# Optimization experiments

Measured on AMD Instinct MI355X. Metric: run time of the kernel, lower is better.

## Reference

```python
import jax, jax.numpy as jnp
from jax import lax
import numpy as np

H = W = 768
N_BOXES = 512
C1, C2 = 32, 64
POOL = 5
NUM_CLASSES = 4
BN_EPS = 1e-5


def setup_inputs() -> dict:
    key = jax.random.key(0)
    ks = jax.random.split(key, 20)
    image = jax.random.normal(ks[0], (1, 3, H, W), jnp.float32)
    # valid boxes: xmax>xmin, ymax>ymin, inside [0, W)
    xmin = jax.random.randint(ks[1], (N_BOXES,), 0, W - 256)
    ymin = jax.random.randint(ks[2], (N_BOXES,), 0, H - 256)
    bw = jax.random.randint(ks[3], (N_BOXES,), 8, 256)
    bh = jax.random.randint(ks[4], (N_BOXES,), 8, 256)
    boxes = jnp.stack([xmin, ymin, xmin + bw, ymin + bh], axis=1).astype(jnp.int32)
    conv1_w = jax.random.normal(ks[5], (C1, 3, 3, 3), jnp.float32) * 0.1
    conv1_b = jax.random.normal(ks[6], (C1,), jnp.float32) * 0.01
    bn1_g = 1.0 + 0.1 * jax.random.normal(ks[7], (C1,), jnp.float32)
    bn1_b = 0.1 * jax.random.normal(ks[8], (C1,), jnp.float32)
    bn1_m = 0.1 * jax.random.normal(ks[9], (C1,), jnp.float32)
    bn1_v = jax.random.uniform(ks[10], (C1,), jnp.float32, 0.5, 1.5)
    conv2_w = jax.random.normal(ks[11], (C2, C1, 3, 3), jnp.float32) * 0.05
    conv2_b = jax.random.normal(ks[12], (C2,), jnp.float32) * 0.01
    bn2_g = 1.0 + 0.1 * jax.random.normal(ks[13], (C2,), jnp.float32)
    bn2_b = 0.1 * jax.random.normal(ks[14], (C2,), jnp.float32)
    bn2_m = 0.1 * jax.random.normal(ks[15], (C2,), jnp.float32)
    bn2_v = jax.random.uniform(ks[16], (C2,), jnp.float32, 0.5, 1.5)
    fc1_w = jax.random.normal(ks[17], (128, C2 * POOL * POOL), jnp.float32) * 0.02
    fc1_b = jnp.zeros((128,), jnp.float32)
    fc2_w = jax.random.normal(ks[18], (NUM_CLASSES, 128), jnp.float32) * 0.05
    fc2_b = jnp.zeros((NUM_CLASSES,), jnp.float32)
    return dict(image=image, boxes=boxes,
                conv1_w=conv1_w, conv1_b=conv1_b, bn1_g=bn1_g, bn1_b=bn1_b, bn1_m=bn1_m, bn1_v=bn1_v,
                conv2_w=conv2_w, conv2_b=conv2_b, bn2_g=bn2_g, bn2_b=bn2_b, bn2_m=bn2_m, bn2_v=bn2_v,
                fc1_w=fc1_w, fc1_b=fc1_b, fc2_w=fc2_w, fc2_b=fc2_b)


def _conv(x, w, b):
    y = lax.conv_general_dilated(x, w, (1, 1), ((1, 1), (1, 1)),
                                 dimension_numbers=("NCHW", "OIHW", "NCHW"))
    return y + b[None, :, None, None]


def _bn(x, g, b, m, v):
    scale = g / jnp.sqrt(v + BN_EPS)
    return x * scale[None, :, None, None] + (b - m * scale)[None, :, None, None]


def _forward(image, boxes, conv1_w, conv1_b, bn1_g, bn1_b, bn1_m, bn1_v,
             conv2_w, conv2_b, bn2_g, bn2_b, bn2_m, bn2_v,
             fc1_w, fc1_b, fc2_w, fc2_b):
    # backbone: Conv -> ReLU -> BN (order as in source), twice
    x = _bn(jax.nn.relu(_conv(image, conv1_w, conv1_b)), bn1_g, bn1_b, bn1_m, bn1_v)
    x = _bn(jax.nn.relu(_conv(x, conv2_w, conv2_b)), bn2_g, bn2_b, bn2_m, bn2_v)
    feat = x[0]  # [C2, H, W], batch assumed 1 as in the per-box slicing loop
    # integral image for exact adaptive-avg-pool over integer index rectangles
    integ = jnp.pad(feat, ((0, 0), (1, 0), (1, 0))).cumsum(1).cumsum(2)  # [C2,H+1,W+1]
    xmin, ymin, xmax, ymax = boxes[:, 0], boxes[:, 1], boxes[:, 2], boxes[:, 3]
    bh = ymax - ymin
    bw = xmax - xmin
    i = jnp.arange(POOL)
    # AdaptiveAvgPool2d bin edges: start=floor(i*L/5), end=ceil((i+1)*L/5)
    y0 = ymin[:, None] + (i * bh[:, None]) // POOL            # [N,5]
    y1 = ymin[:, None] + ((i + 1) * bh[:, None] + POOL - 1) // POOL
    x0 = xmin[:, None] + (i * bw[:, None]) // POOL
    x1 = xmin[:, None] + ((i + 1) * bw[:, None] + POOL - 1) // POOL

    def rect(ys, xs):  # [C2, N, 5, 5]
        return integ[:, ys[:, :, None], xs[:, None, :]]

    s = rect(y1, x1) - rect(y0, x1) - rect(y1, x0) + rect(y0, x0)
    area = ((y1 - y0)[:, :, None] * (x1 - x0)[:, None, :]).astype(feat.dtype)  # [N,5,5]
    pooled = s / area[None]                                    # [C2,N,5,5]
    flat = pooled.transpose(1, 0, 2, 3).reshape(boxes.shape[0], -1)  # [N, C2*25]
    h1 = jax.nn.relu(flat @ fc1_w.T + fc1_b)  # dropout is identity in eval
    return h1 @ fc2_w.T + fc2_b               # [N, num_classes]


def reference(image, boxes, conv1_w, conv1_b, bn1_g, bn1_b, bn1_m, bn1_v,
              conv2_w, conv2_b, bn2_g, bn2_b, bn2_m, bn2_v,
              fc1_w, fc1_b, fc2_w, fc2_b):
    return _forward(image, boxes, conv1_w, conv1_b, bn1_g, bn1_b, bn1_m, bn1_v,
                    conv2_w, conv2_b, bn2_g, bn2_b, bn2_m, bn2_v,
                    fc1_w, fc1_b, fc2_w, fc2_b)
```

## Files before the change

kernel.cpp:

```cpp
#include <hip/hip_runtime.h>
#include <hip/hip_bf16.h>

#define HH 768
#define WW 768
#define HWSZ (HH*WW)
#define BN_EPS 1e-5f
#define SEG 8
#define NSEG 96

typedef __attribute__((ext_vector_type(8))) short bf16x8;
typedef __attribute__((ext_vector_type(4))) float f32x4;

__device__ __forceinline__ float bf2f(unsigned short u) {
  union { unsigned int i; float f; } v; v.i = ((unsigned int)u) << 16; return v.f;
}
__device__ __forceinline__ unsigned short f2bf(float f) {
  union { float f; unsigned int i; } v; v.f = f;
  unsigned int x = v.i;
  return (unsigned short)((x + 0x7fffu + ((x >> 16) & 1u)) >> 16);
}
__device__ __forceinline__ float ldf(const void* p, int i, int flag) {
  return flag ? bf2f(((const unsigned short*)p)[i]) : ((const float*)p)[i];
}

#define DPP_ADD(v, CTRL) do {                                              \
    union { float f; int i; } _u; _u.f = (v);                              \
    int _t = __builtin_amdgcn_update_dpp(0, _u.i, (CTRL), 0xf, 0xf, true); \
    union { int i; float f; } _w; _w.i = _t;                               \
    (v) += _w.f;                                                           \
  } while (0)
__device__ __forceinline__ float row_prefix16(float v) {
  DPP_ADD(v, 0x111);
  DPP_ADD(v, 0x112);
  DPP_ADD(v, 0x114);
  DPP_ADD(v, 0x118);
  return v;
}

__device__ __forceinline__ int detect_flag(const void* v1) {
  const unsigned short* v1raw = (const unsigned short*)v1;
  int ok = 1;
  #pragma unroll
  for (int j = 0; j < 4; ++j) {
    unsigned short u = v1raw[2*j];
    if (u < 0x3E00u || u > 0x4040u) ok = 0;
  }
  return ok;
}

__global__ void k_prep(const void* __restrict__ c1b,
                       const void* __restrict__ g1, const void* __restrict__ b1,
                       const void* __restrict__ m1, const void* __restrict__ v1,
                       const void* __restrict__ c2b, const void* __restrict__ g2,
                       const void* __restrict__ b2, const void* __restrict__ m2,
                       const void* __restrict__ v2, const void* __restrict__ w1,
                       const void* __restrict__ fb1, const void* __restrict__ fw2,
                       const void* __restrict__ fb2, const void* __restrict__ w2,
                       const void* __restrict__ fw1,
                       int* __restrict__ flagp, float* __restrict__ cst,
                       unsigned short* __restrict__ A2, unsigned short* __restrict__ A1,
                       unsigned short* __restrict__ w1c, unsigned int* __restrict__ mask)
{
  int flag = detect_flag(v1);
  int tid = threadIdx.x, bid = blockIdx.x;
  int gid = bid * 256 + tid;

  for (int i = gid; i < 768*24; i += 128*256) mask[i] = 0u;

  if (bid == 0) {
    if (tid == 0) *flagp = flag;
    float* bias1 = cst + 864;
    float* sc1   = cst + 896;
    float* sh1   = cst + 928;
    float* bias2 = cst + 960;
    float* sc2   = cst + 1024;
    float* sh2   = cst + 1088;
    float* fb1c  = cst + 1152;
    float* w2c   = cst + 1280;
    float* fb2c  = cst + 1792;
    if (tid < 32) {
      float s = ldf(g1, tid, flag) * rsqrtf(ldf(v1, tid, flag) + BN_EPS);
      sc1[tid] = s;
      sh1[tid] = ldf(b1, tid, flag) - ldf(m1, tid, flag) * s;
      bias1[tid] = ldf(c1b, tid, flag);
    }
    if (tid < 64) {
      float s = ldf(g2, tid, flag) * rsqrtf(ldf(v2, tid, flag) + BN_EPS);
      sc2[tid] = s;
      sh2[tid] = ldf(b2, tid, flag) - ldf(m2, tid, flag) * s;
      bias2[tid] = ldf(c2b, tid, flag);
    }
    if (tid < 128) fb1c[tid] = ldf(fb1, tid, flag);
    if (tid < 4)   fb2c[tid] = ldf(fb2, tid, flag);
    for (int i = tid; i < 512; i += 256) w2c[i] = ldf(fw2, i, flag);
  }
  if (gid < 80*288) {
    int o = gid / 288, k = gid % 288, tap = k >> 5, ci = k & 31;
    A2[gid] = (o < 64) ? f2bf(ldf(w2, (o*32 + ci)*9 + tap, flag)) : (unsigned short)0;
  }
  if (gid < 32*64) {
    int o = gid >> 6, k = gid & 63, tap = k >> 2, ci = k & 3;
    A1[gid] = (tap < 9 && ci < 3) ? f2bf(ldf(w1, o*27 + ci*9 + tap, flag))
                                  : (unsigned short)0;
  }
  for (int i = gid; i < 128*1600; i += 128*256) {
    int t = i / 1600, r = i % 1600, cell = r >> 6, c = r & 63;
    w1c[i] = f2bf(ldf(fw1, t*1600 + c*25 + cell, flag));
  }
}

__global__ __launch_bounds__(128) void k_mask(const int* __restrict__ boxes,
                                              unsigned int* __restrict__ mask)
{
  int b = blockIdx.x, t = threadIdx.x;
  if (t >= 100) return;
  int a = t / 10, cix = t % 10;
  int xmin = boxes[b*4 + 0], ymin = boxes[b*4 + 1];
  int xmax = boxes[b*4 + 2], ymax = boxes[b*4 + 3];
  int bh = ymax - ymin, bw = xmax - xmin;
  int y, x;
  if (a < 5) y = ymin + ((a+1)*bh + 4)/5 - 1;
  else       y = ymin + ((a-5)*bh)/5 - 1;
  if (cix < 5) x = xmin + ((cix+1)*bw + 4)/5 - 1;
  else         x = xmin + ((cix-5)*bw)/5 - 1;
  if (y >= 0 && x >= 0)
    atomicOr(&mask[y*24 + (x >> 5)], 1u << (x & 31));
}

__global__ __launch_bounds__(256) void k_conv12t(const void* __restrict__ img,
    const int* __restrict__ flagp, const unsigned short* __restrict__ A1,
    const unsigned short* __restrict__ A2, const float* __restrict__ cst,
    const unsigned int* __restrict__ mask, float* __restrict__ T)
{
  const float* bias1 = cst + 864;
  const float* sc1   = cst + 896;
  const float* sh1   = cst + 928;
  const float* bias2 = cst + 960;
  const float* sc2   = cst + 1024;
  const float* sh2   = cst + 1088;
  __shared__ unsigned short ftile[10 * 34 * 40];
  __shared__ unsigned short itile[12 * 36 * 4];
  int flag = *flagp;
  int tid = threadIdx.x;
  int xb = blockIdx.x, ys = blockIdx.y;
  int x0 = xb * 32, ybase = ys * SEG;

  for (int idx = tid; idx < 12*36; idx += 256) {
    int r = idx / 36, p = idx % 36;
    int gy = ybase - 2 + r, gx = x0 - 2 + p;
    unsigned short e0 = 0, e1 = 0, e2 = 0;
    if (gy >= 0 && gy < HH && gx >= 0 && gx < WW) {
      e0 = f2bf(ldf(img, 0*HWSZ + gy*WW + gx, flag));
      e1 = f2bf(ldf(img, 1*HWSZ + gy*WW + gx, flag));
      e2 = f2bf(ldf(img, 2*HWSZ + gy*WW + gx, flag));
    }
    ushort4 pk; pk.x = e0; pk.y = e1; pk.z = e2; pk.w = 0;
    *(ushort4*)(itile + idx*4) = pk;
  }

  int w = tid >> 6, lane = tid & 63, quad = lane >> 4, l16 = lane & 15;

  bf16x8 a1f[2][2];
  #pragma unroll
  for (int mt = 0; mt < 2; ++mt)
    #pragma unroll
    for (int kt = 0; kt < 2; ++kt)
      a1f[mt][kt] = *(const bf16x8*)(A1 + (mt*16 + l16)*64 + kt*32 + quad*8);
  int t0 = 2*quad, t1 = 2*quad + 1;
  int ky0 = t0/3, kx0 = t0%3, ky1 = t1/3, kx1 = t1%3;

  int m = w * 16 + l16;
  bf16x8 afrag[9];
  #pragma unroll
  for (int t = 0; t < 9; ++t)
    afrag[t] = *(const bf16x8*)(A2 + m*288 + t*32 + quad*8);
  float bs[4], scv[4], shv[4];
  #pragma unroll
  for (int r = 0; r < 4; ++r) {
    int c = w*16 + quad*4 + r;
    bs[r] = bias2[c]; scv[r] = sc2[c]; shv[r] = sh2[c];
  }
  __syncthreads();

  for (int u = w; u < 30; u += 4) {
    int r = u / 3, nt = u % 3;
    int pxb = nt*16 + l16;
    int pp = (pxb <= 33) ? pxb : 33;
    union { uint2 q[2]; bf16x8 v; } b0;
    b0.q[0] = *(const uint2*)(itile + ((r + ky0)*36 + pp + kx0)*4);
    b0.q[1] = *(const uint2*)(itile + ((r + ky1)*36 + pp + kx1)*4);
    union { uint2 q[2]; bf16x8 v; } b1v;
    b1v.q[0] = *(const uint2*)(itile + ((r + 2)*36 + pp + 2)*4);
    b1v.q[1] = make_uint2(0u, 0u);
    f32x4 acc[2];
    acc[0] = (f32x4){0.f,0.f,0.f,0.f};
    acc[1] = (f32x4){0.f,0.f,0.f,0.f};
    #pragma unroll
    for (int mt = 0; mt < 2; ++mt) {
      acc[mt] = __builtin_amdgcn_mfma_f32_16x16x32_bf16(a1f[mt][0], b0.v, acc[mt], 0, 0, 0);
      acc[mt] = __builtin_amdgcn_mfma_f32_16x16x32_bf16(a1f[mt][1], b1v.v, acc[mt], 0, 0, 0);
    }
    int py = ybase - 1 + r, gx = x0 - 1 + pxb;
    int inside = (py >= 0 && py < HH && gx >= 0 && gx < WW);
    if (pxb < 34) {
      #pragma unroll
      for (int mt = 0; mt < 2; ++mt) {
        int cb = mt*16 + quad*4;
        ushort4 pk;
        if (inside) {
          pk.x = f2bf(fmaxf(acc[mt][0] + bias1[cb+0], 0.f) * sc1[cb+0] + sh1[cb+0]);
          pk.y = f2bf(fmaxf(acc[mt][1] + bias1[cb+1], 0.f) * sc1[cb+1] + sh1[cb+1]);
          pk.z = f2bf(fmaxf(acc[mt][2] + bias1[cb+2], 0.f) * sc1[cb+2] + sh1[cb+2]);
          pk.w = f2bf(fmaxf(acc[mt][3] + bias1[cb+3], 0.f) * sc1[cb+3] + sh1[cb+3]);
        } else {
          pk.x = pk.y = pk.z = pk.w = 0;
        }
        *(ushort4*)(ftile + (r*34 + pxb)*40 + cb) = pk;
      }
    }
  }
  __syncthreads();

  f32x4 ys0 = (f32x4){0.f,0.f,0.f,0.f};
  f32x4 ys1 = (f32x4){0.f,0.f,0.f,0.f};
  int cbase = w*16 + quad*4;
  for (int dy = 0; dy < SEG; ++dy) {
    int y = ybase + dy;
    f32x4 acc[2];
    acc[0] = (f32x4){0.f,0.f,0.f,0.f};
    acc[1] = (f32x4){0.f,0.f,0.f,0.f};
    #pragma unroll
    for (int t = 0; t < 9; ++t) {
      int ky = t / 3, kx = t % 3;
      #pragma unroll
      for (int i = 0; i < 2; ++i) {
        int px = i*16 + l16 + kx;
        bf16x8 b = *(const bf16x8*)(ftile + ((dy + ky)*34 + px)*40 + quad*8);
        acc[i] = __builtin_amdgcn_mfma_f32_16x16x32_bf16(afrag[t], b, acc[i], 0, 0, 0);
      }
    }
    #pragma unroll
    for (int r = 0; r < 4; ++r) {
      float v0 = fmaxf(acc[0][r] + bs[r], 0.f) * scv[r] + shv[r];
      float v1 = fmaxf(acc[1][r] + bs[r], 0.f) * scv[r] + shv[r];
      v0 = row_prefix16(v0);
      v1 = row_prefix16(v1);
      v1 += __shfl(v0, 15, 16);
      ys0[r] += v0;
      ys1[r] += v1;
    }
    unsigned int mw = mask[y*24 + xb];
    int need0 = (dy == SEG-1) || ((mw >> l16) & 1u);
    int need1 = (dy == SEG-1) || (l16 == 15) || ((mw >> (16 + l16)) & 1u);
    if (need0)
      *(f32x4*)(T + ((size_t)(y*WW + x0 + l16))*64 + cbase)      = ys0;
    if (need1)
      *(f32x4*)(T + ((size_t)(y*WW + x0 + 16 + l16))*64 + cbase) = ys1;
  }
}

__global__ __launch_bounds__(256) void k_cgen(const float* __restrict__ T,
                                              float* __restrict__ C)
{
  __shared__ float Sp[NSEG*24];
  int cc = blockIdx.x, tid = threadIdx.x;
  for (int idx = tid; idx < NSEG*24; idx += 256) {
    int i = idx / 24, j = idx % 24;
    Sp[idx] = T[((size_t)((i*SEG + SEG-1)*WW + j*32 + 31))*64 + cc];
  }
  __syncthreads();
  if (tid < 24) {
    float run = 0.f;
    for (int i = 0; i < NSEG; ++i) { run += Sp[i*24 + tid]; Sp[i*24 + tid] = run; }
  }
  __syncthreads();
  if (tid < NSEG) {
    float run = 0.f;
    #pragma unroll
    for (int j = 0; j < 24; ++j) { run += Sp[tid*24 + j]; Sp[tid*24 + j] = run; }
  }
  __syncthreads();
  for (int idx = tid; idx < NSEG*24; idx += 256)
    C[((size_t)idx)*64 + cc] = Sp[idx];
}

__global__ __launch_bounds__(256) void k_ab(const float* __restrict__ T,
    const float* __restrict__ C, float* __restrict__ A, float* __restrict__ Bp)
{
  __shared__ float gtot[4][64];
  int part = blockIdx.y, tid = threadIdx.x;
  int c = tid & 63, g = tid >> 6;
  if (part == 0) {
    int y = blockIdx.x;
    float vals[6];
    float run = 0.f;
    #pragma unroll
    for (int jj = 0; jj < 6; ++jj) {
      int j = g*6 + jj;
      run += T[((size_t)(y*WW + j*32 + 31))*64 + c];
      vals[jj] = run;
    }
    gtot[g][c] = run;
    __syncthreads();
    float off = 0.f;
    for (int gg = 0; gg < g; ++gg) off += gtot[gg][c];
    #pragma unroll
    for (int jj = 0; jj < 6; ++jj)
      A[((size_t)(y*24 + g*6 + jj))*64 + c] = vals[jj] + off;
  } else {
    int x = blockIdx.x;
    int j = x >> 5;
    float vals[24];
    float run = 0.f;
    #pragma unroll 4
    for (int ii = 0; ii < 24; ++ii) {
      int i = g*24 + ii;
      run += T[((size_t)((i*SEG + SEG-1)*WW + x))*64 + c];
      vals[ii] = run;
    }
    gtot[g][c] = run;
    __syncthreads();
    float off = 0.f;
    for (int gg = 0; gg < g; ++gg) off += gtot[gg][c];
    #pragma unroll 4
    for (int ii = 0; ii < 24; ++ii) {
      int i = g*24 + ii;
      float cj = (j > 0) ? C[((size_t)(i*24 + (j-1)))*64 + c] : 0.f;
      Bp[((size_t)(i*WW + x))*64 + c] = vals[ii] + off + cj;
    }
  }
}

__device__ __forceinline__ float icorner(const float* __restrict__ T,
    const float* __restrict__ A, const float* __restrict__ Bp,
    int c, int yy, int xx)
{
  int i = yy >> 3, j = xx >> 5;
  float v = T[((size_t)(yy*WW + xx))*64 + c];
  if (j > 0) v += A[((size_t)(yy*24 + (j-1)))*64 + c];
  if (i > 0) v += Bp[((size_t)((i-1)*WW + xx))*64 + c];
  return v;
}

__global__ __launch_bounds__(256) void k_roi3(const float* __restrict__ T,
    const float* __restrict__ A, const float* __restrict__ Bp,
    const int* __restrict__ boxes, unsigned short* __restrict__ flat)
{
  int b = blockIdx.x;
  int xmin = boxes[b*4 + 0], ymin = boxes[b*4 + 1];
  int xmax = boxes[b*4 + 2], ymax = boxes[b*4 + 3];
  int bh = ymax - ymin, bw = xmax - xmin;
  for (int idx = threadIdx.x; idx < 1600; idx += 256) {
    int c = idx & 63, cell = idx >> 6, i = cell / 5, j = cell % 5;
    int y0 = ymin + (i*bh)/5,  y1 = ymin + ((i+1)*bh + 4)/5;
    int x0 = xmin + (j*bw)/5,  x1 = xmin + ((j+1)*bw + 4)/5;
    float s = icorner(T, A, Bp, c, y1-1, x1-1);
    if (y0 > 0)           s -= icorner(T, A, Bp, c, y0-1, x1-1);
    if (x0 > 0)           s -= icorner(T, A, Bp, c, y1-1, x0-1);
    if (y0 > 0 && x0 > 0) s += icorner(T, A, Bp, c, y0-1, x0-1);
    float area = (float)((y1 - y0) * (x1 - x0));
    flat[b*1600 + cell*64 + c] = f2bf(s / area);
  }
}

__global__ __launch_bounds__(256) void k_fcm(const unsigned short* __restrict__ flat,
    const unsigned short* __restrict__ w1c, const float* __restrict__ cst,
    const int* __restrict__ flagp, void* __restrict__ out)
{
  const float* fb1c = cst + 1152;
  const float* w2c  = cst + 1280;
  const float* fb2c = cst + 1792;
  __shared__ unsigned short sflat[16 * 1608];
  __shared__ float hbuf[16 * 132];
  int tid = threadIdx.x;
  int b0 = blockIdx.x * 16;
  for (int ii = tid; ii < 3200; ii += 256) {
    int bi = ii / 200, ch = ii % 200;
    *(uint4*)(sflat + bi*1608 + ch*8) = *(const uint4*)(flat + (b0 + bi)*1600 + ch*8);
  }
  __syncthreads();
  int w = tid >> 6, lane = tid & 63, quad = lane >> 4, l16 = lane & 15;
  f32x4 acc[2];
  acc[0] = (f32x4){0.f,0.f,0.f,0.f};
  acc[1] = (f32x4){0.f,0.f,0.f,0.f};
  for (int kt = 0; kt < 50; ++kt) {
    bf16x8 b = *(const bf16x8*)(sflat + l16*1608 + kt*32 + quad*8);
    #pragma unroll
    for (int mt = 0; mt < 2; ++mt) {
      bf16x8 a = *(const bf16x8*)(w1c + ((w*2 + mt)*16 + l16)*1600 + kt*32 + quad*8);
      acc[mt] = __builtin_amdgcn_mfma_f32_16x16x32_bf16(a, b, acc[mt], 0, 0, 0);
    }
  }
  #pragma unroll
  for (int mt = 0; mt < 2; ++mt) {
    #pragma unroll
    for (int r = 0; r < 4; ++r) {
      int h = (w*2 + mt)*16 + quad*4 + r;
      hbuf[l16*132 + h] = fmaxf(acc[mt][r] + fb1c[h], 0.f);
    }
  }
  __syncthreads();
  if (tid < 64) {
    int bi = tid >> 2, o = tid & 3;
    float a2 = fb2c[o];
    for (int k = 0; k < 128; ++k) a2 += hbuf[bi*132 + k] * w2c[o*128 + k];
    if (*flagp) ((unsigned short*)out)[(b0 + bi)*4 + o] = f2bf(a2);
    else        ((float*)out)[(b0 + bi)*4 + o] = a2;
  }
}

__global__ __launch_bounds__(256) void k_conv1m(const void* __restrict__ img,
    const int* __restrict__ flagp, const unsigned short* __restrict__ A1,
    const float* __restrict__ cst, unsigned short* __restrict__ feat1)
{
  const float* bias1 = cst + 864;
  const float* sc1   = cst + 896;
  const float* sh1   = cst + 928;
  int flag = *flagp;
  __shared__ unsigned short tile[18 * 34 * 4];
  int tid = threadIdx.x;
  int x0 = blockIdx.x * 32, ybase = blockIdx.y * 16;
  for (int idx = tid; idx < 18*34; idx += 256) {
    int r = idx / 34, p = idx % 34;
    int gy = ybase - 1 + r, gx = x0 - 1 + p;
    unsigned short e0 = 0, e1 = 0, e2 = 0;
    if (gy >= 0 && gy < HH && gx >= 0 && gx < WW) {
      e0 = f2bf(ldf(img, 0*HWSZ + gy*WW + gx, flag));
      e1 = f2bf(ldf(img, 1*HWSZ + gy*WW + gx, flag));
      e2 = f2bf(ldf(img, 2*HWSZ + gy*WW + gx, flag));
    }
    ushort4 pk; pk.x = e0; pk.y = e1; pk.z = e2; pk.w = 0;
    *(ushort4*)(tile + idx*4) = pk;
  }
  int w = tid >> 6, lane = tid & 63, quad = lane >> 4, l16 = lane & 15;
  bf16x8 a1f[2][2];
  #pragma unroll
  for (int mt = 0; mt < 2; ++mt)
    #pragma unroll
    for (int kt = 0; kt < 2; ++kt)
      a1f[mt][kt] = *(const bf16x8*)(A1 + (mt*16 + l16)*64 + kt*32 + quad*8);
  int t0 = 2*quad, t1 = 2*quad + 1;
  int ky0 = t0/3, kx0 = t0%3, ky1 = t1/3, kx1 = t1%3;
  __syncthreads();
  for (int dyw = 0; dyw < 4; ++dyw) {
    int dy = dyw*4 + w;
    int y = ybase + dy;
    f32x4 acc[2][2];
    #pragma unroll
    for (int mt = 0; mt < 2; ++mt)
      #pragma unroll
      for (int i = 0; i < 2; ++i)
        acc[mt][i] = (f32x4){0.f,0.f,0.f,0.f};
    #pragma unroll
    for (int i = 0; i < 2; ++i) {
      int pxb = i*16 + l16;
      union { uint2 q[2]; bf16x8 v; } b0;
      b0.q[0] = *(const uint2*)(tile + ((dy + ky0)*34 + pxb + kx0)*4);
      b0.q[1] = *(const uint2*)(tile + ((dy + ky1)*34 + pxb + kx1)*4);
      union { uint2 q[2]; bf16x8 v; } b1v;
      b1v.q[0] = *(const uint2*)(tile + ((dy + 2)*34 + pxb + 2)*4);
      b1v.q[1] = make_uint2(0u, 0u);
      #pragma unroll
      for (int mt = 0; mt < 2; ++mt) {
        acc[mt][i] = __builtin_amdgcn_mfma_f32_16x16x32_bf16(a1f[mt][0], b0.v, acc[mt][i], 0, 0, 0);
        acc[mt][i] = __builtin_amdgcn_mfma_f32_16x16x32_bf16(a1f[mt][1], b1v.v, acc[mt][i], 0, 0, 0);
      }
    }
    #pragma unroll
    for (int mt = 0; mt < 2; ++mt) {
      int cb = mt*16 + quad*4;
      #pragma unroll
      for (int i = 0; i < 2; ++i) {
        int px = x0 + i*16 + l16;
        ushort4 pk;
        pk.x = f2bf(fmaxf(acc[mt][i][0] + bias1[cb+0], 0.f) * sc1[cb+0] + sh1[cb+0]);
        pk.y = f2bf(fmaxf(acc[mt][i][1] + bias1[cb+1], 0.f) * sc1[cb+1] + sh1[cb+1]);
        pk.z = f2bf(fmaxf(acc[mt][i][2] + bias1[cb+2], 0.f) * sc1[cb+2] + sh1[cb+2]);
        pk.w = f2bf(fmaxf(acc[mt][i][3] + bias1[cb+3], 0.f) * sc1[cb+3] + sh1[cb+3]);
        *(ushort4*)(feat1 + ((size_t)(y*WW + px))*32 + cb) = pk;
      }
    }
  }
}
__global__ __launch_bounds__(256) void k_conv2_c16(const unsigned short* __restrict__ feat1,
    const unsigned short* __restrict__ A2, const float* __restrict__ cst,
    float* __restrict__ chunk, int c0, int cnw)
{
  const float* bias2 = cst + 960;
  const float* sc2   = cst + 1024;
  const float* sh2   = cst + 1088;
  __shared__ unsigned short tile[3 * 130 * 40];
  int tid = threadIdx.x;
  int y = blockIdx.y, x0 = blockIdx.x * 128;
  for (int idx = tid; idx < 3*130*4; idx += 256) {
    int q = idx & 3, p = (idx >> 2) % 130, r = idx / 520;
    int gy = y - 1 + r, gx = x0 - 1 + p;
    uint4 val = make_uint4(0u, 0u, 0u, 0u);
    if (gy >= 0 && gy < HH && gx >= 0 && gx < WW)
      val = *(const uint4*)(feat1 + (gy*WW + gx)*32 + q*8);
    *(uint4*)(tile + (r*130 + p)*40 + q*8) = val;
  }
  __syncthreads();
  int w = tid >> 6, lane = tid & 63, quad = lane >> 4, l16 = lane & 15;
  int m = c0 + l16;
  f32x4 acc[2];
  acc[0] = (f32x4){0.f,0.f,0.f,0.f};
  acc[1] = (f32x4){0.f,0.f,0.f,0.f};
  #pragma unroll
  for (int t = 0; t < 9; ++t) {
    int ky = t / 3, kx = t % 3;
    bf16x8 a = *(const bf16x8*)(A2 + m*288 + t*32 + quad*8);
    #pragma unroll
    for (int i = 0; i < 2; ++i) {
      int px = w*32 + i*16 + l16 + kx;
      bf16x8 b = *(const bf16x8*)(tile + (ky*130 + px)*40 + quad*8);
      acc[i] = __builtin_amdgcn_mfma_f32_16x16x32_bf16(a, b, acc[i], 0, 0, 0);
    }
  }
  #pragma unroll
  for (int r = 0; r < 4; ++r) {
    int cl = quad*4 + r;
    if (cl < cnw) {
      int c = c0 + cl;
      float bsv = bias2[c], s = sc2[c], sh = sh2[c];
      float* dst = chunk + cl*HWSZ + y*WW;
      #pragma unroll
      for (int i = 0; i < 2; ++i) {
        float v = fmaxf(acc[i][r] + bsv, 0.f) * s + sh;
        dst[x0 + w*32 + i*16 + l16] = v;
      }
    }
  }
}
__global__ __launch_bounds__(256) void k_csy(float* __restrict__ buf) {
  int t = blockIdx.x * 256 + threadIdx.x;
  int c = t / WW, x = t % WW;
  float* p = buf + c*HWSZ + x;
  float run = 0.f;
  for (int yb = 0; yb < HH; yb += 16) {
    float v[16];
    #pragma unroll
    for (int j = 0; j < 16; ++j) v[j] = p[(yb + j) * WW];
    #pragma unroll
    for (int j = 0; j < 16; ++j) { run += v[j]; v[j] = run; }
    #pragma unroll
    for (int j = 0; j < 16; ++j) p[(yb + j) * WW] = v[j];
  }
}
__global__ __launch_bounds__(256) void k_csx(float* __restrict__ buf) {
  int row = blockIdx.x * 4 + (threadIdx.x >> 6);
  int lane = threadIdx.x & 63;
  float* p = buf + (long)row * WW;
  float carry = 0.f;
  for (int ch = 0; ch < 12; ++ch) {
    float v = p[ch*64 + lane];
    #pragma unroll
    for (int off = 1; off < 64; off <<= 1) {
      float t = __shfl_up(v, off);
      v = (lane >= off) ? v + t : v;
    }
    v += carry;
    p[ch*64 + lane] = v;
    carry = __shfl(v, 63);
  }
}
__global__ __launch_bounds__(256) void k_roi(const float* __restrict__ integ,
    const int* __restrict__ boxes, unsigned short* __restrict__ flat, int c0, int cn)
{
  int b = blockIdx.x;
  int xmin = boxes[b*4 + 0], ymin = boxes[b*4 + 1];
  int xmax = boxes[b*4 + 2], ymax = boxes[b*4 + 3];
  int bh = ymax - ymin, bw = xmax - xmin;
  for (int idx = threadIdx.x; idx < cn*25; idx += 256) {
    int cl = idx / 25, cell = idx % 25, i = cell / 5, j = cell % 5;
    int y0 = ymin + (i*bh)/5,      y1 = ymin + ((i+1)*bh + 4)/5;
    int x0 = xmin + (j*bw)/5,      x1 = xmin + ((j+1)*bw + 4)/5;
    const float* I = integ + cl*HWSZ;
    float a  = I[(y1-1)*WW + (x1-1)];
    float bl = (y0 > 0) ? I[(y0-1)*WW + (x1-1)] : 0.f;
    float cr = (x0 > 0) ? I[(y1-1)*WW + (x0-1)] : 0.f;
    float d  = (y0 > 0 && x0 > 0) ? I[(y0-1)*WW + (x0-1)] : 0.f;
    float s = a - bl - cr + d;
    float area = (float)((y1 - y0) * (x1 - x0));
    flat[b*1600 + cell*64 + (c0 + cl)] = f2bf(s / area);
  }
}

extern "C" void kernel_launch(void* const* d_in, const int* in_sizes, int n_in,
                              void* d_out, int out_size, void* d_ws, size_t ws_size,
                              hipStream_t stream) {
  const void* img = d_in[0];
  const int* boxes = (const int*)d_in[1];
  const void* c1w = d_in[2];  const void* c1b = d_in[3];
  const void* g1  = d_in[4];  const void* b1  = d_in[5];
  const void* m1  = d_in[6];  const void* v1  = d_in[7];
  const void* c2w = d_in[8];  const void* c2b = d_in[9];
  const void* g2  = d_in[10]; const void* b2  = d_in[11];
  const void* m2  = d_in[12]; const void* v2  = d_in[13];
  const void* fw1 = d_in[14]; const void* fb1 = d_in[15];
  const void* fw2 = d_in[16]; const void* fb2 = d_in[17];

  char* ws = (char*)d_ws;
  unsigned short* A2 = (unsigned short*)ws;
  unsigned short* A1 = (unsigned short*)(ws + 46080);
  float* cst = (float*)(ws + 50176);
  int* flag = (int*)(ws + 57360);
  unsigned int* mask = (unsigned int*)(ws + 57376);
  unsigned short* w1c  = (unsigned short*)(ws + 3592224);
  unsigned short* flat = (unsigned short*)(ws + 4001824);
  unsigned short* feat1 = (unsigned short*)(ws + 7278624);
  float* T = (float*)(ws + 45027360);
  float* Aarr = (float*)(ws + 7278624);
  float* Bparr = Aarr + (size_t)768*24*64;
  float* Carr = Bparr + (size_t)NSEG*768*64;

  const size_t base = 45027360;
  int cn;
  if      (ws_size >= base + 64ull*HWSZ*4) cn = 64;
  else if (ws_size >= base + 16ull*HWSZ*4) cn = 16;
  else if (ws_size >= base +  8ull*HWSZ*4) cn = 8;
  else if (ws_size >= base +  4ull*HWSZ*4) cn = 4;
  else if (ws_size >= base +  2ull*HWSZ*4) cn = 2;
  else                                     cn = 1;

  hipLaunchKernelGGL(k_prep, dim3(128), dim3(256), 0, stream,
                     c1b, g1, b1, m1, v1, c2b, g2, b2, m2, v2, c1w,
                     fb1, fw2, fb2, c2w, fw1, flag, cst, A2, A1, w1c, mask);

  if (cn == 64) {
    hipLaunchKernelGGL(k_mask, dim3(512), dim3(128), 0, stream, boxes, mask);
    hipLaunchKernelGGL(k_conv12t, dim3(24, NSEG), dim3(256), 0, stream,
                       img, flag, A1, A2, cst, mask, T);
    hipLaunchKernelGGL(k_cgen, dim3(64), dim3(256), 0, stream, T, Carr);
    hipLaunchKernelGGL(k_ab, dim3(768, 2), dim3(256), 0, stream, T, Carr, Aarr, Bparr);
    hipLaunchKernelGGL(k_roi3, dim3(512), dim3(256), 0, stream,
                       T, Aarr, Bparr, boxes, flat);
  } else {
    hipLaunchKernelGGL(k_conv1m, dim3(24, 48), dim3(256), 0, stream,
                       img, flag, A1, cst, feat1);
    for (int c0 = 0; c0 < 64; c0 += cn) {
      hipLaunchKernelGGL(k_conv2_c16, dim3(6, 768), dim3(256), 0, stream,
                         feat1, A2, cst, T, c0, cn);
      hipLaunchKernelGGL(k_csy, dim3(cn*3), dim3(256), 0, stream, T);
      hipLaunchKernelGGL(k_csx, dim3(cn*192), dim3(256), 0, stream, T);
      hipLaunchKernelGGL(k_roi, dim3(512), dim3(256), 0, stream, T, boxes, flat, c0, cn);
    }
  }
  hipLaunchKernelGGL(k_fcm, dim3(32), dim3(256), 0, stream, flat, w1c, cst, flag,
                     d_out);
}
```

Measured before the change: 211.4 us.

## Fuse mask into prep, merge prefix kernels, fuse ROI pooling into FC

Three kernel fusions aim to cut launch count and intermediate traffic. Mask building moves into the prep kernel: a single block builds the bitmask in shared memory with LDS atomics, then copies it out. The C-generation and A/B prefix kernels become one 3-part launch, with the C correction now added in the ROI corner lookup instead of folded into B. ROI pooling is fused into the FC kernel, so the flat buffer round-trip through global memory disappears. The price is that the ROI gather now runs on only 32 blocks instead of 512, and mask building is serialized in one block that uses about 72KB of dynamic shared memory.

```diff
diff --git a/kernel.cpp b/kernel.cpp
--- a/kernel.cpp
+++ b/kernel.cpp
@@ -56,16 +56,15 @@
                        const void* __restrict__ v2, const void* __restrict__ w1,
                        const void* __restrict__ fb1, const void* __restrict__ fw2,
                        const void* __restrict__ fb2, const void* __restrict__ w2,
-                       const void* __restrict__ fw1,
+                       const void* __restrict__ fw1, const int* __restrict__ boxes,
                        int* __restrict__ flagp, float* __restrict__ cst,
                        unsigned short* __restrict__ A2, unsigned short* __restrict__ A1,
                        unsigned short* __restrict__ w1c, unsigned int* __restrict__ mask)
 {
+  extern __shared__ unsigned int smask[];
   int flag = detect_flag(v1);
   int tid = threadIdx.x, bid = blockIdx.x;
   int gid = bid * 256 + tid;
-
-  for (int i = gid; i < 768*24; i += 128*256) mask[i] = 0u;
 
   if (bid == 0) {
     if (tid == 0) *flagp = flag;
@@ -94,6 +93,23 @@
     if (tid < 4)   fb2c[tid] = ldf(fb2, tid, flag);
     for (int i = tid; i < 512; i += 256) w2c[i] = ldf(fw2, i, flag);
   }
+  if (bid == 127) {
+    for (int i = tid; i < 768*24; i += 256) smask[i] = 0u;
+    __syncthreads();
+    for (int u = tid; u < 512*100; u += 256) {
+      int b = u / 100, t = u % 100;
+      int a = t / 10, cix = t % 10;
+      int xmin = boxes[b*4 + 0], ymin = boxes[b*4 + 1];
+      int xmax = boxes[b*4 + 2], ymax = boxes[b*4 + 3];
+      int bh = ymax - ymin, bw = xmax - xmin;
+      int y = (a < 5) ? (ymin + ((a+1)*bh + 4)/5 - 1) : (ymin + ((a-5)*bh)/5 - 1);
+      int x = (cix < 5) ? (xmin + ((cix+1)*bw + 4)/5 - 1) : (xmin + ((cix-5)*bw)/5 - 1);
+      if (y >= 0 && x >= 0)
+        atomicOr(&smask[y*24 + (x >> 5)], 1u << (x & 31));
+    }
+    __syncthreads();
+    for (int i = tid; i < 768*24; i += 256) mask[i] = smask[i];
+  }
   if (gid < 80*288) {
     int o = gid / 288, k = gid % 288, tap = k >> 5, ci = k & 31;
     A2[gid] = (o < 64) ? f2bf(ldf(w2, (o*32 + ci)*9 + tap, flag)) : (unsigned short)0;
@@ -107,24 +123,6 @@
     int t = i / 1600, r = i % 1600, cell = r >> 6, c = r & 63;
     w1c[i] = f2bf(ldf(fw1, t*1600 + c*25 + cell, flag));
   }
-}
-
-__global__ __launch_bounds__(128) void k_mask(const int* __restrict__ boxes,
-                                              unsigned int* __restrict__ mask)
-{
-  int b = blockIdx.x, t = threadIdx.x;
-  if (t >= 100) return;
-  int a = t / 10, cix = t % 10;
-  int xmin = boxes[b*4 + 0], ymin = boxes[b*4 + 1];
-  int xmax = boxes[b*4 + 2], ymax = boxes[b*4 + 3];
-  int bh = ymax - ymin, bw = xmax - xmin;
-  int y, x;
-  if (a < 5) y = ymin + ((a+1)*bh + 4)/5 - 1;
-  else       y = ymin + ((a-5)*bh)/5 - 1;
-  if (cix < 5) x = xmin + ((cix+1)*bw + 4)/5 - 1;
-  else         x = xmin + ((cix-5)*bw)/5 - 1;
-  if (y >= 0 && x >= 0)
-    atomicOr(&mask[y*24 + (x >> 5)], 1u << (x & 31));
 }
 
 __global__ __launch_bounds__(256) void k_conv12t(const void* __restrict__ img,
@@ -259,35 +257,11 @@
   }
 }
 
-__global__ __launch_bounds__(256) void k_cgen(const float* __restrict__ T,
-                                              float* __restrict__ C)
-{
+__global__ __launch_bounds__(256) void k_abc(const float* __restrict__ T,
+    float* __restrict__ A, float* __restrict__ B, float* __restrict__ C)
+{
+  __shared__ float gtot[4][64];
   __shared__ float Sp[NSEG*24];
-  int cc = blockIdx.x, tid = threadIdx.x;
-  for (int idx = tid; idx < NSEG*24; idx += 256) {
-    int i = idx / 24, j = idx % 24;
-    Sp[idx] = T[((size_t)((i*SEG + SEG-1)*WW + j*32 + 31))*64 + cc];
-  }
-  __syncthreads();
-  if (tid < 24) {
-    float run = 0.f;
-    for (int i = 0; i < NSEG; ++i) { run += Sp[i*24 + tid]; Sp[i*24 + tid] = run; }
-  }
-  __syncthreads();
-  if (tid < NSEG) {
-    float run = 0.f;
-    #pragma unroll
-    for (int j = 0; j < 24; ++j) { run += Sp[tid*24 + j]; Sp[tid*24 + j] = run; }
-  }
-  __syncthreads();
-  for (int idx = tid; idx < NSEG*24; idx += 256)
-    C[((size_t)idx)*64 + cc] = Sp[idx];
-}
-
-__global__ __launch_bounds__(256) void k_ab(const float* __restrict__ T,
-    const float* __restrict__ C, float* __restrict__ A, float* __restrict__ Bp)
-{
-  __shared__ float gtot[4][64];
   int part = blockIdx.y, tid = threadIdx.x;
   int c = tid & 63, g = tid >> 6;
   if (part == 0) {
@@ -307,9 +281,8 @@
     #pragma unroll
     for (int jj = 0; jj < 6; ++jj)
       A[((size_t)(y*24 + g*6 + jj))*64 + c] = vals[jj] + off;
-  } else {
+  } else if (part == 1) {
     int x = blockIdx.x;
-    int j = x >> 5;
     float vals[24];
     float run = 0.f;
     #pragma unroll 4
@@ -325,45 +298,47 @@
     #pragma unroll 4
     for (int ii = 0; ii < 24; ++ii) {
       int i = g*24 + ii;
-      float cj = (j > 0) ? C[((size_t)(i*24 + (j-1)))*64 + c] : 0.f;
-      Bp[((size_t)(i*WW + x))*64 + c] = vals[ii] + off + cj;
-    }
-  }
-}
-
-__device__ __forceinline__ float icorner(const float* __restrict__ T,
-    const float* __restrict__ A, const float* __restrict__ Bp,
-    int c, int yy, int xx)
+      B[((size_t)(i*WW + x))*64 + c] = vals[ii] + off;
+    }
+  } else {
+    int cc = blockIdx.x;
+    if (cc >= 64) return;
+    for (int idx = tid; idx < NSEG*24; idx += 256) {
+      int i = idx / 24, j = idx % 24;
+      Sp[idx] = T[((size_t)((i*SEG + SEG-1)*WW + j*32 + 31))*64 + cc];
+    }
+    __syncthreads();
+    if (tid < 24) {
+      float run = 0.f;
+      for (int i = 0; i < NSEG; ++i) { run += Sp[i*24 + tid]; Sp[i*24 + tid] = run; }
+    }
+    __syncthreads();
+    if (tid < NSEG) {
+      float run = 0.f;
+      #pragma unroll
+      for (int j = 0; j < 24; ++j) { run += Sp[tid*24 + j]; Sp[tid*24 + j] = run; }
+    }
+    __syncthreads();
+    for (int idx = tid; idx < NSEG*24; idx += 256)
+      C[((size_t)idx)*64 + cc] = Sp[idx];
+  }
+}
+
+__device__ __forceinline__ float icorner4(const float* __restrict__ T,
+    const float* __restrict__ A, const float* __restrict__ B,
+    const float* __restrict__ C, int c, int yy, int xx)
 {
   int i = yy >> 3, j = xx >> 5;
   float v = T[((size_t)(yy*WW + xx))*64 + c];
   if (j > 0) v += A[((size_t)(yy*24 + (j-1)))*64 + c];
-  if (i > 0) v += Bp[((size_t)((i-1)*WW + xx))*64 + c];
+  if (i > 0) v += B[((size_t)((i-1)*WW + xx))*64 + c];
+  if (i > 0 && j > 0) v += C[((size_t)((i-1)*24 + (j-1)))*64 + c];
   return v;
 }
 
-__global__ __launch_bounds__(256) void k_roi3(const float* __restrict__ T,
-    const float* __restrict__ A, const float* __restrict__ Bp,
-    const int* __restrict__ boxes, unsigned short* __restrict__ flat)
-{
-  int b = blockIdx.x;
-  int xmin = boxes[b*4 + 0], ymin = boxes[b*4 + 1];
-  int xmax = boxes[b*4 + 2], ymax = boxes[b*4 + 3];
-  int bh = ymax - ymin, bw = xmax - xmin;
-  for (int idx = threadIdx.x; idx < 1600; idx += 256) {
-    int c = idx & 63, cell = idx >> 6, i = cell / 5, j = cell % 5;
-    int y0 = ymin + (i*bh)/5,  y1 = ymin + ((i+1)*bh + 4)/5;
-    int x0 = xmin + (j*bw)/5,  x1 = xmin + ((j+1)*bw + 4)/5;
-    float s = icorner(T, A, Bp, c, y1-1, x1-1);
-    if (y0 > 0)           s -= icorner(T, A, Bp, c, y0-1, x1-1);
-    if (x0 > 0)           s -= icorner(T, A, Bp, c, y1-1, x0-1);
-    if (y0 > 0 && x0 > 0) s += icorner(T, A, Bp, c, y0-1, x0-1);
-    float area = (float)((y1 - y0) * (x1 - x0));
-    flat[b*1600 + cell*64 + c] = f2bf(s / area);
-  }
-}
-
-__global__ __launch_bounds__(256) void k_fcm(const unsigned short* __restrict__ flat,
+__global__ __launch_bounds__(256) void k_roifc(const float* __restrict__ T,
+    const float* __restrict__ A, const float* __restrict__ B,
+    const float* __restrict__ C, const int* __restrict__ boxes,
     const unsigned short* __restrict__ w1c, const float* __restrict__ cst,
     const int* __restrict__ flagp, void* __restrict__ out)
 {
@@ -374,11 +349,25 @@
   __shared__ float hbuf[16 * 132];
   int tid = threadIdx.x;
   int b0 = blockIdx.x * 16;
-  for (int ii = tid; ii < 3200; ii += 256) {
-    int bi = ii / 200, ch = ii % 200;
-    *(uint4*)(sflat + bi*1608 + ch*8) = *(const uint4*)(flat + (b0 + bi)*1600 + ch*8);
-  }
-  __syncthreads();
+
+  for (int u = tid; u < 16*1600; u += 256) {
+    int bi = u / 1600, r = u % 1600;
+    int c = r & 63, cell = r >> 6, i = cell / 5, j = cell % 5;
+    int bb = b0 + bi;
+    int xmin = boxes[bb*4 + 0], ymin = boxes[bb*4 + 1];
+    int xmax = boxes[bb*4 + 2], ymax = boxes[bb*4 + 3];
+    int bh = ymax - ymin, bw = xmax - xmin;
+    int y0 = ymin + (i*bh)/5,  y1 = ymin + ((i+1)*bh + 4)/5;
+    int x0 = xmin + (j*bw)/5,  x1 = xmin + ((j+1)*bw + 4)/5;
+    float s = icorner4(T, A, B, C, c, y1-1, x1-1);
+    if (y0 > 0)           s -= icorner4(T, A, B, C, c, y0-1, x1-1);
+    if (x0 > 0)           s -= icorner4(T, A, B, C, c, y1-1, x0-1);
+    if (y0 > 0 && x0 > 0) s += icorner4(T, A, B, C, c, y0-1, x0-1);
+    float area = (float)((y1 - y0) * (x1 - x0));
+    sflat[bi*1608 + cell*64 + c] = f2bf(s / area);
+  }
+  __syncthreads();
+
   int w = tid >> 6, lane = tid & 63, quad = lane >> 4, l16 = lane & 15;
   f32x4 acc[2];
   acc[0] = (f32x4){0.f,0.f,0.f,0.f};
@@ -585,6 +574,51 @@
     flat[b*1600 + cell*64 + (c0 + cl)] = f2bf(s / area);
   }
 }
+__global__ __launch_bounds__(256) void k_fcm(const unsigned short* __restrict__ flat,
+    const unsigned short* __restrict__ w1c, const float* __restrict__ cst,
+    const int* __restrict__ flagp, void* __restrict__ out)
+{
+  const float* fb1c = cst + 1152;
+  const float* w2c  = cst + 1280;
+  const float* fb2c = cst + 1792;
+  __shared__ unsigned short sflat[16 * 1608];
+  __shared__ float hbuf[16 * 132];
+  int tid = threadIdx.x;
+  int b0 = blockIdx.x * 16;
+  for (int ii = tid; ii < 3200; ii += 256) {
+    int bi = ii / 200, ch = ii % 200;
+    *(uint4*)(sflat + bi*1608 + ch*8) = *(const uint4*)(flat + (b0 + bi)*1600 + ch*8);
+  }
+  __syncthreads();
+  int w = tid >> 6, lane = tid & 63, quad = lane >> 4, l16 = lane & 15;
+  f32x4 acc[2];
+  acc[0] = (f32x4){0.f,0.f,0.f,0.f};
+  acc[1] = (f32x4){0.f,0.f,0.f,0.f};
+  for (int kt = 0; kt < 50; ++kt) {
+    bf16x8 b = *(const bf16x8*)(sflat + l16*1608 + kt*32 + quad*8);
+    #pragma unroll
+    for (int mt = 0; mt < 2; ++mt) {
+      bf16x8 a = *(const bf16x8*)(w1c + ((w*2 + mt)*16 + l16)*1600 + kt*32 + quad*8);
+      acc[mt] = __builtin_amdgcn_mfma_f32_16x16x32_bf16(a, b, acc[mt], 0, 0, 0);
+    }
+  }
+  #pragma unroll
+  for (int mt = 0; mt < 2; ++mt) {
+    #pragma unroll
+    for (int r = 0; r < 4; ++r) {
+      int h = (w*2 + mt)*16 + quad*4 + r;
+      hbuf[l16*132 + h] = fmaxf(acc[mt][r] + fb1c[h], 0.f);
+    }
+  }
+  __syncthreads();
+  if (tid < 64) {
+    int bi = tid >> 2, o = tid & 3;
+    float a2 = fb2c[o];
+    for (int k = 0; k < 128; ++k) a2 += hbuf[bi*132 + k] * w2c[o*128 + k];
+    if (*flagp) ((unsigned short*)out)[(b0 + bi)*4 + o] = f2bf(a2);
+    else        ((float*)out)[(b0 + bi)*4 + o] = a2;
+  }
+}
 
 extern "C" void kernel_launch(void* const* d_in, const int* in_sizes, int n_in,
                               void* d_out, int out_size, void* d_ws, size_t ws_size,
@@ -611,8 +645,8 @@
   unsigned short* feat1 = (unsigned short*)(ws + 7278624);
   float* T = (float*)(ws + 45027360);
   float* Aarr = (float*)(ws + 7278624);
-  float* Bparr = Aarr + (size_t)768*24*64;
-  float* Carr = Bparr + (size_t)NSEG*768*64;
+  float* Barr = Aarr + (size_t)768*24*64;
+  float* Carr = Barr + (size_t)NSEG*768*64;
 
   const size_t base = 45027360;
   int cn;
@@ -623,18 +657,17 @@
   else if (ws_size >= base +  2ull*HWSZ*4) cn = 2;
   else                                     cn = 1;
 
-  hipLaunchKernelGGL(k_prep, dim3(128), dim3(256), 0, stream,
+  hipLaunchKernelGGL(k_prep, dim3(128), dim3(256), 768*24*4, stream,
                      c1b, g1, b1, m1, v1, c2b, g2, b2, m2, v2, c1w,
-                     fb1, fw2, fb2, c2w, fw1, flag, cst, A2, A1, w1c, mask);
+                     fb1, fw2, fb2, c2w, fw1, boxes, flag, cst, A2, A1, w1c, mask);
 
   if (cn == 64) {
-    hipLaunchKernelGGL(k_mask, dim3(512), dim3(128), 0, stream, boxes, mask);
     hipLaunchKernelGGL(k_conv12t, dim3(24, NSEG), dim3(256), 0, stream,
                        img, flag, A1, A2, cst, mask, T);
-    hipLaunchKernelGGL(k_cgen, dim3(64), dim3(256), 0, stream, T, Carr);
-    hipLaunchKernelGGL(k_ab, dim3(768, 2), dim3(256), 0, stream, T, Carr, Aarr, Bparr);
-    hipLaunchKernelGGL(k_roi3, dim3(512), dim3(256), 0, stream,
-                       T, Aarr, Bparr, boxes, flat);
+    hipLaunchKernelGGL(k_abc, dim3(768, 3), dim3(256), 0, stream,
+                       T, Aarr, Barr, Carr);
+    hipLaunchKernelGGL(k_roifc, dim3(32), dim3(256), 0, stream,
+                       T, Aarr, Barr, Carr, boxes, w1c, cst, flag, d_out);
   } else {
     hipLaunchKernelGGL(k_conv1m, dim3(24, 48), dim3(256), 0, stream,
                        img, flag, A1, cst, feat1);
@@ -645,7 +678,7 @@
       hipLaunchKernelGGL(k_csx, dim3(cn*192), dim3(256), 0, stream, T);
       hipLaunchKernelGGL(k_roi, dim3(512), dim3(256), 0, stream, T, boxes, flat, c0, cn);
     }
-  }
-  hipLaunchKernelGGL(k_fcm, dim3(32), dim3(256), 0, stream, flat, w1c, cst, flag,
-                     d_out);
-}
+    hipLaunchKernelGGL(k_fcm, dim3(32), dim3(256), 0, stream, flat, w1c, cst, flag,
+                       d_out);
+  }
+}
```

After: 541.8 us. 2.56x slower.
